# Kernel optimization log

Measured on AMD Instinct MI355X. Metric: run time of the kernel, lower is better.

The kernel has to match this reference:

```python
import jax, jax.numpy as jnp
import numpy as np

SEQ_LEN = 256
DT = 0.05
PI4 = float(np.pi / 4)
B = 16384


def _policy(h, W1, b1, W2, b2, W3, b3, W4, b4):
    h = jax.nn.relu(h @ W1 + b1)
    h = jax.nn.relu(h @ W2 + b2)
    h = jax.nn.relu(h @ W3 + b3)
    return jnp.tanh(h @ W4 + b4)


def setup_inputs() -> dict:
    key = jax.random.key(0)
    ks = jax.random.split(key, 11)
    return {
        "state": jax.random.normal(ks[0], (B, 6), jnp.float32),
        "pstate": jax.random.normal(ks[1], (B, 6), jnp.float32),
        "target": jax.random.normal(ks[2], (B, 6), jnp.float32),
        "W1": jax.random.normal(ks[3], (12, 50), jnp.float32) * 0.2,
        "b1": jax.random.normal(ks[4], (50,), jnp.float32) * 0.1,
        "W2": jax.random.normal(ks[5], (50, 50), jnp.float32) * 0.14,
        "b2": jax.random.normal(ks[6], (50,), jnp.float32) * 0.1,
        "W3": jax.random.normal(ks[7], (50, 50), jnp.float32) * 0.14,
        "b3": jax.random.normal(ks[8], (50,), jnp.float32) * 0.1,
        "W4": jax.random.normal(ks[9], (50, 2), jnp.float32) * 0.14,
        "b4": jax.random.normal(ks[10], (2,), jnp.float32) * 0.1,
    }


def reference(state, pstate, target, W1, b1, W2, b2, W3, b3, W4, b4):
    # target duplicated to match concat(pstate, state): [B, 12]
    tgt = jnp.concatenate([target, target], axis=-1)

    def step(carry, _):
        pstate, state = carry
        u = _policy(jnp.concatenate([pstate, state], axis=-1) - tgt,
                    W1, b1, W2, b2, W3, b3, W4, b4) * 0.5  # [B, 2]
        x, y, c, s, v, w = (state[:, i] for i in range(6))
        cw = jnp.cos(w * DT)
        sw = jnp.sin(w * DT)
        x = x + v * c * DT
        y = y + v * s * DT
        c_new = c * cw - s * sw
        # NOTE: original torch code uses the *updated* c when updating s
        s_new = s * cw + c_new * sw
        v = jnp.clip(v + u[:, 0] * DT, -0.1, 0.3)
        w = jnp.clip(w + u[:, 1] * DT, -PI4, PI4)
        new_state = jnp.stack([x, y, c_new, s_new, v, w], axis=-1)
        return (state, new_state), (u, new_state)

    _, (u_seq, states) = jax.lax.scan(step, (pstate, state), None, length=SEQ_LEN)
    # u_seq: [SEQ_LEN, B, 2], states: [SEQ_LEN, B, 6]
    return u_seq, states
```

## Files before the change

### kernel.cpp

```cpp
#include <hip/hip_runtime.h>
#include <hip/hip_bf16.h>
#include <stdint.h>
#include <math.h>

#define SEQ_LEN 256
#define BATCH   16384

typedef _Float16 half8  __attribute__((ext_vector_type(8)));
typedef _Float16 half2t __attribute__((ext_vector_type(2)));
typedef __attribute__((ext_vector_type(4))) float    floatx4;
typedef __attribute__((ext_vector_type(4))) uint32_t uint4v;
typedef __attribute__((ext_vector_type(2))) float    float2v;

__device__ __forceinline__ uint32_t pkh(float a, float b){
    return __builtin_bit_cast(uint32_t, __builtin_amdgcn_cvt_pkrtz(a, b));
}
__device__ __forceinline__ float h16lo(uint32_t p){
    return (float)__builtin_bit_cast(half2t, p)[0];
}
__device__ __forceinline__ float h16hi(uint32_t p){
    return (float)__builtin_bit_cast(half2t, p)[1];
}
__device__ __forceinline__ uint32_t pkh_rne(float a, float b){
    uint32_t ua = (uint32_t)__builtin_bit_cast(unsigned short, (_Float16)a);
    uint32_t ub = (uint32_t)__builtin_bit_cast(unsigned short, (_Float16)b);
    return ua | (ub << 16);
}
__device__ __forceinline__ half8 ashfrag(uint4v u){ return __builtin_bit_cast(half8, u); }
#define MFMA_H(A,B,C) __builtin_amdgcn_mfma_f32_16x16x32_f16((A),(B),(C),0,0,0)

__global__ __launch_bounds__(64, 1) void mbrl_mfma(
    const float* __restrict__ state0, const float* __restrict__ pstate0,
    const float* __restrict__ target,
    const float* __restrict__ W1, const float* __restrict__ b1,
    const float* __restrict__ W2, const float* __restrict__ b2,
    const float* __restrict__ W3, const float* __restrict__ b3,
    const float* __restrict__ W4, const float* __restrict__ b4,
    float* __restrict__ out)
{
    const int lane = threadIdx.x & 63;
    const int c16  = lane & 15;
    const int phi  = lane >> 4;
    const int rowg = (int)blockIdx.x * 16 + c16;

    half8 P1[4], Q1[4];
#pragma unroll
    for (int t = 0; t < 4; ++t){
        const int j = 16*t + c16;
        uint4v uP, uQ;
#pragma unroll
        for (int v = 0; v < 4; ++v){
            float pP[2], pQ[2];
#pragma unroll
            for (int q = 0; q < 2; ++q){
                const int kk = 16*(v>>1) + 4*phi + 2*(v&1) + q;
                float w = 0.f;
                if (j < 50){
                    if (kk < 12)                  w = W1[kk*50 + j];
                    else if (kk == 12)            w = b1[j];
                    else if (kk >= 16 && kk < 28) w = W1[(kk-16)*50 + j];
                }
                float s0 = (float)(_Float16)w;
                pP[q] = s0; pQ[q] = w - s0;
            }
            uP[v] = pkh(pP[0], pP[1]);
            uQ[v] = pkh(pQ[0], pQ[1]);
        }
        P1[t] = ashfrag(uP); Q1[t] = ashfrag(uQ);
    }

    half8 A2[2][4][2], A3[2][4][2];
#pragma unroll
    for (int t = 0; t < 4; ++t){
        const int j = 16*t + c16;
#pragma unroll
        for (int kt = 0; kt < 2; ++kt){
            uint4v u2[2], u3[2];
#pragma unroll
            for (int v = 0; v < 4; ++v){
                float p2[2][2], p3[2][2];
#pragma unroll
                for (int q = 0; q < 2; ++q){
                    const int kk = 32*kt + 16*(v>>1) + 4*phi + 2*(v&1) + q;
                    float w2v = 0.f, w3v = 0.f;
                    if (j < 50){
                        if (kk < 50){ w2v = W2[kk*50 + j]; w3v = W3[kk*50 + j]; }
                        else if (kk == 50){ w2v = b2[j]; w3v = b3[j]; }
                    }
                    float a0  = (float)(_Float16)w2v;
                    float c0s = (float)(_Float16)w3v;
                    p2[0][q] = a0;  p2[1][q] = w2v - a0;
                    p3[0][q] = c0s; p3[1][q] = w3v - c0s;
                }
#pragma unroll
                for (int s = 0; s < 2; ++s){
                    u2[s][v] = pkh(p2[s][0], p2[s][1]);
                    u3[s][v] = pkh(p3[s][0], p3[s][1]);
                }
            }
#pragma unroll
            for (int s = 0; s < 2; ++s){
                A2[s][t][kt] = ashfrag(u2[s]); A3[s][t][kt] = ashfrag(u3[s]);
            }
        }
    }

    float w4a[16], w4b[16];
#pragma unroll
    for (int t = 0; t < 4; ++t)
#pragma unroll
        for (int r = 0; r < 4; ++r){
            const int j = 16*t + 4*phi + r;
            w4a[4*t+r] = (j < 50) ? W4[j*2 + 0] : 0.f;
            w4b[4*t+r] = (j < 50) ? W4[j*2 + 1] : 0.f;
        }
    const float b40 = b4[0], b41 = b4[1];

    float ss[6];
#pragma unroll
    for (int i = 0; i < 6; ++i) ss[i] = state0[(size_t)rowg*6 + i];

    float tgs0, tgs1, tgs2, tgs3;
    {
        const float* tg = target + (size_t)rowg*6;
        tgs0 = (phi==0) ? tg[0] : (phi==1) ? tg[4] : (phi==2) ? tg[2] : 0.f;
        tgs1 = (phi==0) ? tg[1] : (phi==1) ? tg[5] : (phi==2) ? tg[3] : 0.f;
        tgs2 = (phi==0) ? tg[2] : (phi==1) ? tg[0] : (phi==2) ? tg[4] : 0.f;
        tgs3 = (phi==0) ? tg[3] : (phi==1) ? tg[1] : (phi==2) ? tg[5] : 0.f;
    }
    float a0, a1, a2, a3;
    {
        const float* ps0 = pstate0 + (size_t)rowg*6;
        a0 = (phi==0) ? ps0[0] : (phi==1) ? ps0[4] : (phi==2) ? ss[2] : 0.f;
        a1 = (phi==0) ? ps0[1] : (phi==1) ? ps0[5] : (phi==2) ? ss[3] : 0.f;
        a2 = (phi==0) ? ps0[2] : (phi==1) ? ss[0]  : (phi==2) ? ss[4] : 0.f;
        a3 = (phi==0) ? ps0[3] : (phi==1) ? ss[1]  : (phi==2) ? ss[5] : 0.f;
    }

    const float DT  = 0.05f;
    const float PI4 = 0.78539816339744830962f;
    const floatx4 z4 = {0.f,0.f,0.f,0.f};
    const uint32_t ONE_H = 0x00003C00u;

    float* uout = out + (size_t)rowg * 2;
    float* sout = out + (size_t)SEQ_LEN * BATCH * 2 + (size_t)rowg * 6;

    half8 H0a, H0b;

#define SPLITH(HA,HB,PK0,PK1) do{                                      \
        PK0 = pkh((HA),(HB));                                          \
        float _a = h16lo(PK0), _b = h16hi(PK0);                        \
        PK1 = pkh((HA)-_a, (HB)-_b);                                   \
    }while(0)

#define MKH(cc0,cc1,cc2,cc3) do{                                                   \
        uint4v u0a, u0b;                                                           \
        u0a[0] = pkh_rne(fmaxf(cc0[0],0.f), fmaxf(cc0[1],0.f));                    \
        u0a[1] = pkh_rne(fmaxf(cc0[2],0.f), fmaxf(cc0[3],0.f));                    \
        u0a[2] = pkh_rne(fmaxf(cc1[0],0.f), fmaxf(cc1[1],0.f));                    \
        u0a[3] = pkh_rne(fmaxf(cc1[2],0.f), fmaxf(cc1[3],0.f));                    \
        u0b[0] = pkh_rne(fmaxf(cc2[0],0.f), fmaxf(cc2[1],0.f));                    \
        u0b[1] = pkh_rne(fmaxf(cc2[2],0.f), fmaxf(cc2[3],0.f));                    \
        u0b[2] = pkh_rne(fmaxf(cc3[0],0.f), fmaxf(cc3[1],0.f));                    \
        u0b[3] = pkh_rne(fmaxf(cc3[2],0.f), fmaxf(cc3[3],0.f));                    \
        if (phi == 0) u0b[3] = ONE_H;                        \
        H0a = ashfrag(u0a); H0b = ashfrag(u0b);                                    \
    }while(0)

#define HID_RR(A)                                                                            \
        c0=MFMA_H(A[0][0][0],H0a,z4); c1=MFMA_H(A[0][1][0],H0a,z4); c2=MFMA_H(A[0][2][0],H0a,z4); c3=MFMA_H(A[0][3][0],H0a,z4); \
        c0=MFMA_H(A[0][0][1],H0b,c0); c1=MFMA_H(A[0][1][1],H0b,c1); c2=MFMA_H(A[0][2][1],H0b,c2); c3=MFMA_H(A[0][3][1],H0b,c3); \
        c0=MFMA_H(A[1][0][0],H0a,c0); c1=MFMA_H(A[1][1][0],H0a,c1); c2=MFMA_H(A[1][2][0],H0a,c2); c3=MFMA_H(A[1][3][0],H0a,c3); \
        c0=MFMA_H(A[1][0][1],H0b,c0); c1=MFMA_H(A[1][1][1],H0b,c1); c2=MFMA_H(A[1][2][1],H0b,c2); c3=MFMA_H(A[1][3][1],H0b,c3);

#define L4ACC(CT,T) do{                                                   \
        _Pragma("unroll")                                                 \
        for (int r = 0; r < 4; ++r){                                      \
            float hv = fmaxf(CT[r], 0.f);                                 \
            z0p = fmaf(hv, w4a[4*(T)+r], z0p);                            \
            z1p = fmaf(hv, w4b[4*(T)+r], z1p);                            \
        }                                                                 \
    }while(0)

    for (int t = 0; t < SEQ_LEN; ++t){
        float xs0 = a0 - tgs0, xs1 = a1 - tgs1;
        float xs2 = a2 - tgs2, xs3 = a3 - tgs3;
        uint32_t pH01,pL01,pH23,pL23;
        SPLITH(xs0,xs1,pH01,pL01);
        SPLITH(xs2,xs3,pH23,pL23);
        uint4v f1;
        f1[0] = (phi==3) ? ONE_H : pH01;
        f1[1] = pH23;
        f1[2] = pL01;
        f1[3] = pL23;
        const half8 F1 = ashfrag(f1);

        floatx4 c0, c1, c2, c3;
        c0=MFMA_H(P1[0],F1,z4); c1=MFMA_H(P1[1],F1,z4); c2=MFMA_H(P1[2],F1,z4); c3=MFMA_H(P1[3],F1,z4);
        c0=MFMA_H(Q1[0],F1,c0); c1=MFMA_H(Q1[1],F1,c1); c2=MFMA_H(Q1[2],F1,c2); c3=MFMA_H(Q1[3],F1,c3);
        MKH(c0,c1,c2,c3);

        HID_RR(A2)
        MKH(c0,c1,c2,c3);

        HID_RR(A3)

        float z0p = 0.f, z1p = 0.f;
        L4ACC(c0,0); L4ACC(c1,1); L4ACC(c2,2); L4ACC(c3,3);
        z0p += __shfl_xor(z0p, 16, 64);
        z1p += __shfl_xor(z1p, 16, 64);
        z0p += __shfl_xor(z0p, 32, 64);
        z1p += __shfl_xor(z1p, 32, 64);
        float zz0 = z0p + b40;
        float zz1 = z1p + b41;

        float u0 = 0.5f - __builtin_amdgcn_rcpf(__expf(2.0f*zz0) + 1.0f);
        float u1 = 0.5f - __builtin_amdgcn_rcpf(__expf(2.0f*zz1) + 1.0f);

        float th = ss[5]*DT, t2 = th*th;
        float sw = th * fmaf(t2, fmaf(t2, 8.3333333333e-3f, -1.6666666667e-1f), 1.0f);
        float cw = fmaf(t2, fmaf(t2, fmaf(t2, -1.3888888889e-3f, 4.1666666667e-2f), -0.5f), 1.0f);
        float nx = fmaf(ss[4]*ss[2], DT, ss[0]);
        float ny = fmaf(ss[4]*ss[3], DT, ss[1]);
        float nc = ss[2]*cw - ss[3]*sw;
        float ns = fmaf(ss[3], cw, nc*sw);
        float nv = fminf(fmaxf(fmaf(u0, DT, ss[4]), -0.1f), 0.3f);
        float nw = fminf(fmaxf(fmaf(u1, DT, ss[5]), -PI4), PI4);

        if (phi == 0){
            float2v uv  = {u0, u1};
            *(float2v*)uout = uv;
            float2v s01 = {nx, ny}, s23 = {nc, ns}, s45 = {nv, nw};
            *(float2v*)(sout    ) = s01;
            *(float2v*)(sout + 2) = s23;
            *(float2v*)(sout + 4) = s45;
        }
        uout += (size_t)BATCH * 2;
        sout += (size_t)BATCH * 6;

        a0 = (phi==0) ? ss[0] : (phi==1) ? ss[4] : (phi==2) ? nc : a0;
        a1 = (phi==0) ? ss[1] : (phi==1) ? ss[5] : (phi==2) ? ns : a1;
        a2 = (phi==0) ? ss[2] : (phi==1) ? nx    : (phi==2) ? nv : a2;
        a3 = (phi==0) ? ss[3] : (phi==1) ? ny    : (phi==2) ? nw : a3;

        ss[0]=nx; ss[1]=ny; ss[2]=nc; ss[3]=ns; ss[4]=nv; ss[5]=nw;
    }
#undef MKH
#undef SPLITH
#undef HID_RR
#undef L4ACC
}

extern "C" void kernel_launch(void* const* d_in, const int* in_sizes, int n_in,
                              void* d_out, int out_size, void* d_ws, size_t ws_size,
                              hipStream_t stream)
{
    const float* state  = (const float*)d_in[0];
    const float* pstate = (const float*)d_in[1];
    const float* target = (const float*)d_in[2];
    const float* W1 = (const float*)d_in[3];
    const float* b1 = (const float*)d_in[4];
    const float* W2 = (const float*)d_in[5];
    const float* b2 = (const float*)d_in[6];
    const float* W3 = (const float*)d_in[7];
    const float* b3 = (const float*)d_in[8];
    const float* W4 = (const float*)d_in[9];
    const float* b4 = (const float*)d_in[10];
    float* out = (float*)d_out;

    dim3 grid(BATCH/16), block(64);
    mbrl_mfma<<<grid, block, 0, stream>>>(state, pstate, target,
                                          W1,b1,W2,b2,W3,b3,W4,b4, out);
}
```

Before: 237.3 us.

## Precompute next-step layer-1 MFMA off critical path, correct v/w terms in FP32

Layer-1 contributions from the inputs that are known early (positions, orientation, previous state) are computed one step ahead with MFMA, overlapping the layer-4 reduction and tanh. The velocity and angular-velocity inputs, which depend on the current policy output, are added afterwards as a rank-2 FP32 FMA correction using preloaded W1 rows 10 and 11. Cross-lane reductions use permlane16/32 swap builtins when available instead of DPP/ds shuffles. This shortens the serial dependency chain per timestep but adds registers and slightly changes how those two features are rounded (FP32 instead of split FP16).

After: 236.1 us. About the same (-0.5%).

```diff
diff --git a/kernel.cpp b/kernel.cpp
--- a/kernel.cpp
+++ b/kernel.cpp
@@ -28,6 +28,25 @@
 }
 __device__ __forceinline__ half8 ashfrag(uint4v u){ return __builtin_bit_cast(half8, u); }
 #define MFMA_H(A,B,C) __builtin_amdgcn_mfma_f32_16x16x32_f16((A),(B),(C),0,0,0)
+
+__device__ __forceinline__ float xor16_sum(float z){
+#if __has_builtin(__builtin_amdgcn_permlane16_swap)
+    uint32_t u = __builtin_bit_cast(uint32_t, z);
+    auto p = __builtin_amdgcn_permlane16_swap(u, u, false, false);
+    return __builtin_bit_cast(float, (uint32_t)p[0]) + __builtin_bit_cast(float, (uint32_t)p[1]);
+#else
+    return z + __shfl_xor(z, 16, 64);
+#endif
+}
+__device__ __forceinline__ float xor32_sum(float z){
+#if __has_builtin(__builtin_amdgcn_permlane32_swap)
+    uint32_t u = __builtin_bit_cast(uint32_t, z);
+    auto p = __builtin_amdgcn_permlane32_swap(u, u, false, false);
+    return __builtin_bit_cast(float, (uint32_t)p[0]) + __builtin_bit_cast(float, (uint32_t)p[1]);
+#else
+    return z + __shfl_xor(z, 32, 64);
+#endif
+}
 
 __global__ __launch_bounds__(64, 1) void mbrl_mfma(
     const float* __restrict__ state0, const float* __restrict__ pstate0,
@@ -116,26 +135,40 @@
         }
     const float b40 = b4[0], b41 = b4[1];
 
+    float wc10[16], wc11[16];
+#pragma unroll
+    for (int t = 0; t < 4; ++t)
+#pragma unroll
+        for (int r = 0; r < 4; ++r){
+            const int j = 16*t + 4*phi + r;
+            wc10[4*t+r] = (j < 50) ? W1[10*50 + j] : 0.f;
+            wc11[4*t+r] = (j < 50) ? W1[11*50 + j] : 0.f;
+        }
+
     float ss[6];
 #pragma unroll
     for (int i = 0; i < 6; ++i) ss[i] = state0[(size_t)rowg*6 + i];
+
+    const float tg4 = target[(size_t)rowg*6 + 4];
+    const float tg5 = target[(size_t)rowg*6 + 5];
 
     float tgs0, tgs1, tgs2, tgs3;
     {
         const float* tg = target + (size_t)rowg*6;
         tgs0 = (phi==0) ? tg[0] : (phi==1) ? tg[4] : (phi==2) ? tg[2] : 0.f;
         tgs1 = (phi==0) ? tg[1] : (phi==1) ? tg[5] : (phi==2) ? tg[3] : 0.f;
-        tgs2 = (phi==0) ? tg[2] : (phi==1) ? tg[0] : (phi==2) ? tg[4] : 0.f;
-        tgs3 = (phi==0) ? tg[3] : (phi==1) ? tg[1] : (phi==2) ? tg[5] : 0.f;
+        tgs2 = (phi==0) ? tg[2] : (phi==1) ? tg[0] : 0.f;
+        tgs3 = (phi==0) ? tg[3] : (phi==1) ? tg[1] : 0.f;
     }
     float a0, a1, a2, a3;
     {
         const float* ps0 = pstate0 + (size_t)rowg*6;
         a0 = (phi==0) ? ps0[0] : (phi==1) ? ps0[4] : (phi==2) ? ss[2] : 0.f;
         a1 = (phi==0) ? ps0[1] : (phi==1) ? ps0[5] : (phi==2) ? ss[3] : 0.f;
-        a2 = (phi==0) ? ps0[2] : (phi==1) ? ss[0]  : (phi==2) ? ss[4] : 0.f;
-        a3 = (phi==0) ? ps0[3] : (phi==1) ? ss[1]  : (phi==2) ? ss[5] : 0.f;
-    }
+        a2 = (phi==0) ? ps0[2] : (phi==1) ? ss[0]  : 0.f;
+        a3 = (phi==0) ? ps0[3] : (phi==1) ? ss[1]  : 0.f;
+    }
+    float cv = ss[4], cvw = ss[5];
 
     const float DT  = 0.05f;
     const float PI4 = 0.78539816339744830962f;
@@ -151,6 +184,20 @@
         PK0 = pkh((HA),(HB));                                          \
         float _a = h16lo(PK0), _b = h16hi(PK0);                        \
         PK1 = pkh((HA)-_a, (HB)-_b);                                   \
+    }while(0)
+
+#define BUILD_F1(F) do{                                                \
+        float xs0 = a0 - tgs0, xs1 = a1 - tgs1;                        \
+        float xs2 = a2 - tgs2, xs3 = a3 - tgs3;                        \
+        uint32_t pH01,pL01,pH23,pL23;                                  \
+        SPLITH(xs0,xs1,pH01,pL01);                                     \
+        SPLITH(xs2,xs3,pH23,pL23);                                     \
+        uint4v f1;                                                     \
+        f1[0] = (phi==3) ? ONE_H : pH01;                               \
+        f1[1] = pH23;                                                  \
+        f1[2] = pL01;                                                  \
+        f1[3] = pL23;                                                  \
+        F = ashfrag(f1);                                               \
     }while(0)
 
 #define MKH(cc0,cc1,cc2,cc3) do{                                                   \
@@ -182,40 +229,30 @@
         }                                                                 \
     }while(0)
 
+#define CORR(CT,T) do{                                                    \
+        _Pragma("unroll")                                                 \
+        for (int r = 0; r < 4; ++r)                                       \
+            CT[r] = fmaf(wc10[4*(T)+r], xv, fmaf(wc11[4*(T)+r], xw, CT[r])); \
+    }while(0)
+
+    half8 F1;
+    BUILD_F1(F1);
+    floatx4 d0, d1, d2, d3;
+    d0=MFMA_H(P1[0],F1,z4); d1=MFMA_H(P1[1],F1,z4); d2=MFMA_H(P1[2],F1,z4); d3=MFMA_H(P1[3],F1,z4);
+    d0=MFMA_H(Q1[0],F1,d0); d1=MFMA_H(Q1[1],F1,d1); d2=MFMA_H(Q1[2],F1,d2); d3=MFMA_H(Q1[3],F1,d3);
+
     for (int t = 0; t < SEQ_LEN; ++t){
-        float xs0 = a0 - tgs0, xs1 = a1 - tgs1;
-        float xs2 = a2 - tgs2, xs3 = a3 - tgs3;
-        uint32_t pH01,pL01,pH23,pL23;
-        SPLITH(xs0,xs1,pH01,pL01);
-        SPLITH(xs2,xs3,pH23,pL23);
-        uint4v f1;
-        f1[0] = (phi==3) ? ONE_H : pH01;
-        f1[1] = pH23;
-        f1[2] = pL01;
-        f1[3] = pL23;
-        const half8 F1 = ashfrag(f1);
-
-        floatx4 c0, c1, c2, c3;
-        c0=MFMA_H(P1[0],F1,z4); c1=MFMA_H(P1[1],F1,z4); c2=MFMA_H(P1[2],F1,z4); c3=MFMA_H(P1[3],F1,z4);
-        c0=MFMA_H(Q1[0],F1,c0); c1=MFMA_H(Q1[1],F1,c1); c2=MFMA_H(Q1[2],F1,c2); c3=MFMA_H(Q1[3],F1,c3);
+        floatx4 c0 = d0, c1 = d1, c2 = d2, c3 = d3;
+        {
+            float xv = cv - tg4, xw = cvw - tg5;
+            CORR(c0,0); CORR(c1,1); CORR(c2,2); CORR(c3,3);
+        }
         MKH(c0,c1,c2,c3);
 
         HID_RR(A2)
         MKH(c0,c1,c2,c3);
 
         HID_RR(A3)
-
-        float z0p = 0.f, z1p = 0.f;
-        L4ACC(c0,0); L4ACC(c1,1); L4ACC(c2,2); L4ACC(c3,3);
-        z0p += __shfl_xor(z0p, 16, 64);
-        z1p += __shfl_xor(z1p, 16, 64);
-        z0p += __shfl_xor(z0p, 32, 64);
-        z1p += __shfl_xor(z1p, 32, 64);
-        float zz0 = z0p + b40;
-        float zz1 = z1p + b41;
-
-        float u0 = 0.5f - __builtin_amdgcn_rcpf(__expf(2.0f*zz0) + 1.0f);
-        float u1 = 0.5f - __builtin_amdgcn_rcpf(__expf(2.0f*zz1) + 1.0f);
 
         float th = ss[5]*DT, t2 = th*th;
         float sw = th * fmaf(t2, fmaf(t2, 8.3333333333e-3f, -1.6666666667e-1f), 1.0f);
@@ -224,6 +261,25 @@
         float ny = fmaf(ss[4]*ss[3], DT, ss[1]);
         float nc = ss[2]*cw - ss[3]*sw;
         float ns = fmaf(ss[3], cw, nc*sw);
+
+        a0 = (phi==0) ? ss[0] : (phi==1) ? ss[4] : (phi==2) ? nc : a0;
+        a1 = (phi==0) ? ss[1] : (phi==1) ? ss[5] : (phi==2) ? ns : a1;
+        a2 = (phi==0) ? ss[2] : (phi==1) ? nx    : a2;
+        a3 = (phi==0) ? ss[3] : (phi==1) ? ny    : a3;
+        BUILD_F1(F1);
+        d0=MFMA_H(P1[0],F1,z4); d1=MFMA_H(P1[1],F1,z4); d2=MFMA_H(P1[2],F1,z4); d3=MFMA_H(P1[3],F1,z4);
+        d0=MFMA_H(Q1[0],F1,d0); d1=MFMA_H(Q1[1],F1,d1); d2=MFMA_H(Q1[2],F1,d2); d3=MFMA_H(Q1[3],F1,d3);
+
+        float z0p = 0.f, z1p = 0.f;
+        L4ACC(c0,0); L4ACC(c1,1); L4ACC(c2,2); L4ACC(c3,3);
+        z0p = xor16_sum(z0p); z1p = xor16_sum(z1p);
+        z0p = xor32_sum(z0p); z1p = xor32_sum(z1p);
+        float zz0 = z0p + b40;
+        float zz1 = z1p + b41;
+
+        float u0 = 0.5f - __builtin_amdgcn_rcpf(__expf(2.0f*zz0) + 1.0f);
+        float u1 = 0.5f - __builtin_amdgcn_rcpf(__expf(2.0f*zz1) + 1.0f);
+
         float nv = fminf(fmaxf(fmaf(u0, DT, ss[4]), -0.1f), 0.3f);
         float nw = fminf(fmaxf(fmaf(u1, DT, ss[5]), -PI4), PI4);
 
@@ -238,17 +294,15 @@
         uout += (size_t)BATCH * 2;
         sout += (size_t)BATCH * 6;
 
-        a0 = (phi==0) ? ss[0] : (phi==1) ? ss[4] : (phi==2) ? nc : a0;
-        a1 = (phi==0) ? ss[1] : (phi==1) ? ss[5] : (phi==2) ? ns : a1;
-        a2 = (phi==0) ? ss[2] : (phi==1) ? nx    : (phi==2) ? nv : a2;
-        a3 = (phi==0) ? ss[3] : (phi==1) ? ny    : (phi==2) ? nw : a3;
-
+        cv = nv; cvw = nw;
         ss[0]=nx; ss[1]=ny; ss[2]=nc; ss[3]=ns; ss[4]=nv; ss[5]=nw;
     }
 #undef MKH
 #undef SPLITH
+#undef BUILD_F1
 #undef HID_RR
 #undef L4ACC
+#undef CORR
 }
 
 extern "C" void kernel_launch(void* const* d_in, const int* in_sizes, int n_in,
```
